# Optimization experiments

Hardware: AMD Instinct MI355X
Metric: run time of the kernel (lower is better)

## Reference

```python
import jax, jax.numpy as jnp
import numpy as np

N0, N1, N2 = 100000, 25000, 6250
F = 128
OUT = 5


def _mean_agg(feat_src, src, dst, n_dst):
    # DGL copy_u + mean: segment mean over destination nodes (0 for isolated dst)
    s = jax.ops.segment_sum(feat_src[src], dst, num_segments=n_dst)
    cnt = jax.ops.segment_sum(jnp.ones_like(dst, dtype=feat_src.dtype), dst, num_segments=n_dst)
    return s / jnp.maximum(cnt, 1.0)[:, None]


def _graph_conv(feat, src, dst, W, b, n):
    # DGL GraphConv, norm='both': D_src^-1/2 gather-sum D_dst^-1/2, then linear
    dt = feat.dtype
    out_deg = jax.ops.segment_sum(jnp.ones_like(src, dtype=dt), src, num_segments=n)
    in_deg = jax.ops.segment_sum(jnp.ones_like(dst, dtype=dt), dst, num_segments=n)
    ns = jnp.where(out_deg > 0, out_deg ** -0.5, 0.0)
    nd = jnp.where(in_deg > 0, in_deg ** -0.5, 0.0)
    agg = jax.ops.segment_sum((feat * ns[:, None])[src], dst, num_segments=n)
    return (agg * nd[:, None]) @ W + b


def setup_inputs() -> dict:
    key = jax.random.key(0)
    keys = jax.random.split(key, 64)
    _c = iter(range(64))
    def nrm(shape, s=0.05):
        return jax.random.normal(keys[next(_c)], shape, dtype=jnp.float32) * s
    def ri(n, hi):
        return jax.random.randint(keys[next(_c)], (n,), 0, hi)
    inp = {
        'X': nrm((N0, 32), 1.0),
        'g0_src': ri(1600000, N0), 'g0_dst': ri(1600000, N0),
        'g1_src': ri(400000, N1), 'g1_dst': ri(400000, N1),
        'g2_src': ri(100000, N2), 'g2_dst': ri(100000, N2),
        'inc0_src': ri(100000, N0), 'inc0_dst': ri(100000, N1),
        'inc1_src': ri(25000, N1), 'inc1_dst': ri(25000, N2),
        'dec0_src': ri(100000, N2), 'dec0_dst': ri(100000, N1),
        'dec1_src': ri(400000, N1), 'dec1_dst': ri(400000, N0),
        'W_emb': nrm((32, F)), 'b_emb': jnp.zeros((F,), jnp.float32),
        'W_gcn0': nrm((F, F)), 'b_gcn0': jnp.zeros((F,), jnp.float32),
        'W_gcn1': nrm((F, F)), 'b_gcn1': jnp.zeros((F,), jnp.float32),
        'W_gcn2': nrm((F, F)), 'b_gcn2': jnp.zeros((F,), jnp.float32),
        'W_enc0': nrm((F, F)), 'b_enc0': jnp.zeros((F,), jnp.float32),
        'W_enc1': nrm((F, F)), 'b_enc1': jnp.zeros((F,), jnp.float32),
        'W_dec0': nrm((F, F)), 'b_dec0': jnp.zeros((F,), jnp.float32),
        'W_dec1': nrm((F, F)), 'b_dec1': jnp.zeros((F,), jnp.float32),
        'W_head0': nrm((2 * F, OUT)), 'b_head0': jnp.zeros((OUT,), jnp.float32),
        'W_head1': nrm((2 * F, OUT)), 'b_head1': jnp.zeros((OUT,), jnp.float32),
        'W_head2': nrm((2 * F, OUT)), 'b_head2': jnp.zeros((OUT,), jnp.float32),
    }
    return inp


def reference(X, g0_src, g0_dst, g1_src, g1_dst, g2_src, g2_dst,
              inc0_src, inc0_dst, inc1_src, inc1_dst,
              dec0_src, dec0_dst, dec1_src, dec1_dst,
              W_emb, b_emb, W_gcn0, b_gcn0, W_gcn1, b_gcn1, W_gcn2, b_gcn2,
              W_enc0, b_enc0, W_enc1, b_enc1, W_dec0, b_dec0, W_dec1, b_dec1,
              W_head0, b_head0, W_head1, b_head1, W_head2, b_head2):
    # embedding at finest scale
    h0 = X @ W_emb + b_emb                                   # [N0, F]
    # encode + pool fine -> coarse (copy_u/mean)
    h1 = _mean_agg(h0 @ W_enc0 + b_enc0, inc0_src, inc0_dst, N1)   # [N1, F]
    h2 = _mean_agg(h1 @ W_enc1 + b_enc1, inc1_src, inc1_dst, N2)   # [N2, F]
    # intra-scale GraphConv
    g0 = _graph_conv(h0, g0_src, g0_dst, W_gcn0, b_gcn0, N0)
    g1 = _graph_conv(h1, g1_src, g1_dst, W_gcn1, b_gcn1, N1)
    g2 = _graph_conv(h2, g2_src, g2_dst, W_gcn2, b_gcn2, N2)
    # decode coarse -> fine
    d2 = g2
    d1 = _mean_agg(d2 @ W_dec0 + b_dec0, dec0_src, dec0_dst, N1)   # [N1, F]
    d0 = _mean_agg(d1 @ W_dec1 + b_dec1, dec1_src, dec1_dst, N0)   # [N0, F]
    # per-scale heads with softmax
    o0 = jax.nn.softmax(jnp.concatenate([g0, d0], -1) @ W_head0 + b_head0, axis=-1)
    o1 = jax.nn.softmax(jnp.concatenate([g1, d1], -1) @ W_head1 + b_head1, axis=-1)
    o2 = jax.nn.softmax(jnp.concatenate([g2, d2], -1) @ W_head2 + b_head2, axis=-1)
    return jnp.concatenate([o0, o1, o2], axis=0)             # [N0+N1+N2, OUT]
```

## Files before the change

### kernel.cpp

```cpp
#include <hip/hip_runtime.h>

#define F 128
static const int N0 = 100000, N1 = 25000, N2 = 6250;

typedef unsigned short u16;
typedef unsigned int   u32;
typedef __attribute__((ext_vector_type(8))) short bf16x8;
typedef __attribute__((ext_vector_type(4))) float f32x4;

__device__ __forceinline__ float bf2f(u16 u) {
    union { u32 i; float f; } v; v.i = ((u32)u) << 16; return v.f;
}
__device__ __forceinline__ u16 f2bf(float f) {
    u32 u = __float_as_uint(f);
    u += 0x7fff + ((u >> 16) & 1);
    return (u16)(u >> 16);
}

struct Seg7 {
    const int* src[7];
    const int* dst[7];
    int end[7];
    int cbase[7];
    int obase[7];
};

#define EPT 4
#define CEPT 8
#define SM32  (64*(32+8)*2 + 128*(32+8)*2 + 128*4)
#define SM128 (64*(128+8)*2 + 128*(128+8)*2 + 128*4)


template <int K, bool AF32, bool MASK>
__device__ __forceinline__ void dev_mm(char* smem, const void* __restrict__ Ap,
                                       const float* __restrict__ W,
                                       const float* __restrict__ bias,
                                       u16* __restrict__ out,
                                       const int* __restrict__ rowptr,
                                       int M, int blk) {
    const int AST = K + 8;
    const int WST = K + 8;
    u16* Al = (u16*)smem;
    u16* Wt = (u16*)(smem + 64 * AST * 2);
    float* bl = (float*)(smem + 64 * AST * 2 + 128 * WST * 2);
    int tid = threadIdx.x;
    int m0 = blk * 64;

    for (int i = tid; i < K * 128; i += 256) {
        int k = i >> 7, n = i & 127;
        Wt[n * WST + k] = f2bf(W[i]);
    }
    for (int i = tid; i < 64 * K; i += 256) {
        int r = i / K, c = i % K;
        int gr = m0 + r;
        u16 v = 0;
        if (gr < M) {
            if (AF32) v = f2bf(((const float*)Ap)[(size_t)gr * K + c]);
            else      v = ((const u16*)Ap)[(size_t)gr * K + c];
        }
        Al[r * AST + c] = v;
    }
    if (tid < 128) bl[tid] = bias[tid];
    __syncthreads();

    int w = tid >> 6;
    int lane = tid & 63;
    int m16 = lane & 15;
    int quad = lane >> 4;

    f32x4 acc[8];
#pragma unroll
    for (int t = 0; t < 8; t++)
#pragma unroll
        for (int r = 0; r < 4; r++) acc[t][r] = 0.f;

    for (int k0 = 0; k0 < K; k0 += 32) {
        bf16x8 af = *(const bf16x8*)&Al[(w * 16 + m16) * AST + k0 + quad * 8];
#pragma unroll
        for (int t = 0; t < 8; t++) {
            bf16x8 bf = *(const bf16x8*)&Wt[(t * 16 + m16) * WST + k0 + quad * 8];
            acc[t] = __builtin_amdgcn_mfma_f32_16x16x32_bf16(af, bf, acc[t], 0, 0, 0);
        }
    }

#pragma unroll
    for (int t = 0; t < 8; t++) {
#pragma unroll
        for (int r = 0; r < 4; r++) {
            int gr = m0 + w * 16 + quad * 4 + r;
            if (gr >= M) continue;
            int gc = t * 16 + m16;
            bool zrow = false;
            if (MASK) zrow = (rowptr[gr + 1] == rowptr[gr]);
            float v = acc[t][r] + bl[gc];
            out[(size_t)gr * F + gc] = zrow ? (u16)0 : f2bf(v);
        }
    }
}

template <int MODE>
__device__ __forceinline__ void dev_gather(const u16* __restrict__ feat,
                                           const int* __restrict__ rowptr,
                                           const int* __restrict__ col,
                                           const int* __restrict__ od,
                                           u16* __restrict__ out, int M, int blk) {
    int wv = (blk * 256 + (int)threadIdx.x) >> 6;
    if (wv >= M) return;
    int lane = threadIdx.x & 63;
    int fo = lane << 1;
    int beg = rowptr[wv], end = rowptr[wv + 1];
    float a0 = 0.f, a1 = 0.f;
    int j = beg;
    for (; j + 8 <= end; j += 8) {
        int cc[8];
#pragma unroll
        for (int t = 0; t < 8; t++) cc[t] = col[j + t];
        float ss[8];
#pragma unroll
        for (int t = 0; t < 8; t++) {
            if (MODE == 1) { int o = od[cc[t]]; ss[t] = o > 0 ? rsqrtf((float)o) : 0.f; }
            else ss[t] = 1.f;
        }
        ushort2 uu[8];
#pragma unroll
        for (int t = 0; t < 8; t++) uu[t] = *(const ushort2*)&feat[(size_t)cc[t] * F + fo];
#pragma unroll
        for (int t = 0; t < 8; t++) { a0 += bf2f(uu[t].x) * ss[t]; a1 += bf2f(uu[t].y) * ss[t]; }
    }
    for (; j < end; j++) {
        int c = col[j];
        float s = 1.f;
        if (MODE == 1) { int o = od[c]; s = o > 0 ? rsqrtf((float)o) : 0.f; }
        ushort2 u = *(const ushort2*)&feat[(size_t)c * F + fo];
        a0 += bf2f(u.x) * s; a1 += bf2f(u.y) * s;
    }
    int deg = end - beg;
    float fs = (MODE == 0) ? (deg > 0 ? 1.f / (float)deg : 0.f)
                           : (deg > 0 ? rsqrtf((float)deg) : 0.f);
    ushort2 o; o.x = f2bf(a0 * fs); o.y = f2bf(a1 * fs);
    *(ushort2*)&out[(size_t)wv * F + fo] = o;
}

template <bool GD>
__device__ __forceinline__ void dev_head(char* smem, const u16* __restrict__ g,
                                         const u16* __restrict__ d,
                                         const int* __restrict__ rowptr,
                                         const int* __restrict__ col,
                                         const float* __restrict__ Wh,
                                         const float* __restrict__ bh,
                                         float* __restrict__ out, int M, int blk) {
    float* Wl = (float*)smem;
    float* bl = (float*)(smem + 1280 * 4);
    int tid = threadIdx.x;
    for (int i = tid; i < 1280; i += 256) Wl[i] = Wh[i];
    if (tid < 5) bl[tid] = bh[tid];
    __syncthreads();

    int lane = tid & 63;
    int wv = tid >> 6;
    int r0 = blk * 32 + wv * 8;
    int k0 = lane << 1;
    for (int i = 0; i < 8; i++) {
        int row = r0 + i;
        if (row < M) {
            float d0v, d1v;
            if (GD) {
                int beg = rowptr[row], end = rowptr[row + 1];
                d0v = 0.f; d1v = 0.f;
                int j = beg;
                for (; j + 4 <= end; j += 4) {
                    int c0 = col[j], c1 = col[j + 1], c2 = col[j + 2], c3 = col[j + 3];
                    ushort2 u0 = *(const ushort2*)&d[(size_t)c0 * F + k0];
                    ushort2 u1 = *(const ushort2*)&d[(size_t)c1 * F + k0];
                    ushort2 u2 = *(const ushort2*)&d[(size_t)c2 * F + k0];
                    ushort2 u3 = *(const ushort2*)&d[(size_t)c3 * F + k0];
                    d0v += bf2f(u0.x) + bf2f(u1.x) + bf2f(u2.x) + bf2f(u3.x);
                    d1v += bf2f(u0.y) + bf2f(u1.y) + bf2f(u2.y) + bf2f(u3.y);
                }
                for (; j < end; j++) {
                    int c = col[j];
                    ushort2 u = *(const ushort2*)&d[(size_t)c * F + k0];
                    d0v += bf2f(u.x); d1v += bf2f(u.y);
                }
                int deg = end - beg;
                float fs = deg > 0 ? 1.f / (float)deg : 0.f;
                d0v *= fs; d1v *= fs;
            } else {
                ushort2 du = *(const ushort2*)&d[(size_t)row * F + k0];
                d0v = bf2f(du.x); d1v = bf2f(du.y);
            }
            ushort2 gu = *(const ushort2*)&g[(size_t)row * F + k0];
            float g0v = bf2f(gu.x), g1v = bf2f(gu.y);
            float p[5];
#pragma unroll
            for (int o = 0; o < 5; o++) {
                p[o] = g0v * Wl[k0 * 5 + o] + g1v * Wl[(k0 + 1) * 5 + o] +
                       d0v * Wl[(k0 + 128) * 5 + o] + d1v * Wl[(k0 + 129) * 5 + o];
            }
#pragma unroll
            for (int o = 0; o < 5; o++) {
                float v = p[o];
                v += __shfl_xor(v, 32, 64);
                v += __shfl_xor(v, 16, 64);
                v += __shfl_xor(v, 8, 64);
                v += __shfl_xor(v, 4, 64);
                v += __shfl_xor(v, 2, 64);
                v += __shfl_xor(v, 1, 64);
                p[o] = v + bl[o];
            }
            if (lane == 0) {
                float m = p[0];
#pragma unroll
                for (int o = 1; o < 5; o++) m = fmaxf(m, p[o]);
                float e[5], s = 0.f;
#pragma unroll
                for (int o = 0; o < 5; o++) { e[o] = expf(p[o] - m); s += e[o]; }
                float inv = 1.f / s;
#pragma unroll
                for (int o = 0; o < 5; o++) out[(size_t)row * 5 + o] = e[o] * inv;
            }
        }
    }
}


__global__ __launch_bounds__(256) void k_count_emb(Seg7 S, int* __restrict__ cnt,
                                                   u16* __restrict__ occ, int ETOT,
                                                   const float* __restrict__ X,
                                                   const float* __restrict__ Wemb,
                                                   const float* __restrict__ bemb,
                                                   u16* __restrict__ h0, int nbMM) {
    __shared__ char smem[SM32];
    if ((int)blockIdx.x < nbMM) {
        dev_mm<32, true, false>(smem, X, Wemb, bemb, h0, nullptr, N0, blockIdx.x);
        return;
    }
    int base = ((int)blockIdx.x - nbMM) * (256 * CEPT) + threadIdx.x;
    int ee[CEPT], grow[CEPT];
#pragma unroll
    for (int t = 0; t < CEPT; t++) {
        int e = base + t * 256;
        ee[t] = e;
        grow[t] = -1;
        if (e < ETOT) {
            int s = 0;
            while (e >= S.end[s]) s++;
            int le = e - ((s == 0) ? 0 : S.end[s - 1]);
            grow[t] = S.cbase[s] + S.dst[s][le];
        }
    }
    u32 r[CEPT];
#pragma unroll
    for (int t = 0; t < CEPT; t++)
        if (grow[t] >= 0) r[t] = atomicAdd((u32*)&cnt[grow[t]], 1u);
#pragma unroll
    for (int t = 0; t < CEPT; t++)
        if (grow[t] >= 0) occ[ee[t]] = (u16)r[t];
}

__global__ __launch_bounds__(256) void k_fill_od(Seg7 S,
                                                 const int* __restrict__ rowptr,
                                                 const u16* __restrict__ occ,
                                                 int* __restrict__ col,
                                                 int* __restrict__ od, int ETOT,
                                                 float invRow, float invOd) {
    int win = blockIdx.x & 7;
    int base = ((int)blockIdx.x >> 3) * (256 * EPT) + threadIdx.x;
#pragma unroll
    for (int t = 0; t < EPT; t++) {
        int e = base + t * 256;
        if (e >= ETOT) break;
        int s = 0;
        while (e >= S.end[s]) s++;
        int le = e - ((s == 0) ? 0 : S.end[s - 1]);
        int grow = S.cbase[s] + S.dst[s][le];
        int w1 = (int)((float)grow * invRow); w1 = w1 > 7 ? 7 : w1;
        int sv = -1;
        if (w1 == win || S.obase[s] >= 0) sv = S.src[s][le];
        if (w1 == win) col[rowptr[grow] + (int)occ[e]] = sv;
        if (S.obase[s] >= 0) {
            int gs = S.obase[s] + sv;
            int w2 = (int)((float)gs * invOd); w2 = w2 > 7 ? 7 : w2;
            if (w2 == win) atomicAdd(&od[gs], 1);
        }
    }
}

#define SCHUNK 4096
__global__ __launch_bounds__(1024) void k_scan1(const int* __restrict__ cnt,
                                                int* __restrict__ partial, int n) {
    __shared__ int red[1024];
    int tid = threadIdx.x;
    int base = blockIdx.x * SCHUNK + tid * 4;
    int s = 0;
#pragma unroll
    for (int j = 0; j < 4; j++) { int i = base + j; if (i < n) s += cnt[i]; }
    red[tid] = s;
    __syncthreads();
    for (int d = 512; d > 0; d >>= 1) {
        if (tid < d) red[tid] += red[tid + d];
        __syncthreads();
    }
    if (tid == 0) partial[blockIdx.x] = red[0];
}

__global__ __launch_bounds__(128) void k_scan2(int* __restrict__ partial, int G) {
    __shared__ int sh[128];
    int tid = threadIdx.x;
    sh[tid] = (tid < G) ? partial[tid] : 0;
    __syncthreads();
    for (int d = 1; d < 128; d <<= 1) {
        int t = (tid >= d) ? sh[tid - d] : 0;
        __syncthreads();
        sh[tid] += t;
        __syncthreads();
    }
    if (tid < G) partial[tid] = (tid > 0) ? sh[tid - 1] : 0;
    if (tid == 127) partial[G] = sh[127];
}

__global__ __launch_bounds__(1024) void k_scan3(const int* __restrict__ cnt,
                                                const int* __restrict__ partial,
                                                int* __restrict__ rowptr,
                                                int n, int G) {
    __shared__ int red[1024];
    int tid = threadIdx.x;
    int base = blockIdx.x * SCHUNK + tid * 4;
    int v0 = 0, v1 = 0, v2 = 0, v3 = 0;
    if (base + 0 < n) v0 = cnt[base + 0];
    if (base + 1 < n) v1 = cnt[base + 1];
    if (base + 2 < n) v2 = cnt[base + 2];
    if (base + 3 < n) v3 = cnt[base + 3];
    red[tid] = v0 + v1 + v2 + v3;
    __syncthreads();
    for (int d = 1; d < 1024; d <<= 1) {
        int t = (tid >= d) ? red[tid - d] : 0;
        __syncthreads();
        red[tid] += t;
        __syncthreads();
    }
    int off = partial[blockIdx.x] + ((tid > 0) ? red[tid - 1] : 0);
    if (base + 0 < n) { rowptr[base + 0] = off; off += v0; }
    if (base + 1 < n) { rowptr[base + 1] = off; off += v1; }
    if (base + 2 < n) { rowptr[base + 2] = off; off += v2; }
    if (base + 3 < n) { rowptr[base + 3] = off; off += v3; }
    if (blockIdx.x == 0 && tid == 0) rowptr[n] = partial[G];
}

template <int MODE>
__global__ __launch_bounds__(256) void k_gather(const u16* __restrict__ feat,
                                                const int* __restrict__ rowptr,
                                                const int* __restrict__ col,
                                                const int* __restrict__ od,
                                                u16* __restrict__ out, int M) {
    dev_gather<MODE>(feat, rowptr, col, od, out, M, blockIdx.x);
}

template <int K, bool AF32, bool MASK>
__global__ __launch_bounds__(256) void k_mm(const void* __restrict__ Ap,
                                            const float* __restrict__ W,
                                            const float* __restrict__ bias,
                                            u16* __restrict__ out,
                                            const int* __restrict__ rowptr,
                                            int M) {
    __shared__ char smem[K == 32 ? SM32 : SM128];
    dev_mm<K, AF32, MASK>(smem, Ap, W, bias, out, rowptr, M, blockIdx.x);
}

template <int MA, int MB>
__global__ __launch_bounds__(256) void k_gather2(
    const u16* fA, const int* rpA, const int* oA, u16* outA, int MAr, int nbA,
    const u16* fB, const int* rpB, const int* oB, u16* outB, int MBr,
    const int* __restrict__ col) {
    if ((int)blockIdx.x < nbA) dev_gather<MA>(fA, rpA, col, oA, outA, MAr, blockIdx.x);
    else                       dev_gather<MB>(fB, rpB, col, oB, outB, MBr, blockIdx.x - nbA);
}

__global__ __launch_bounds__(256) void k_mm2(
    const u16* A1, const float* W1, const float* b1, u16* o1, const int* rp1, int M1, int nb1,
    const u16* A2, const float* W2, const float* b2, u16* o2, int M2) {
    __shared__ char smem[SM128];
    if ((int)blockIdx.x < nb1) dev_mm<128, false, true >(smem, A1, W1, b1, o1, rp1, M1, blockIdx.x);
    else                       dev_mm<128, false, false>(smem, A2, W2, b2, o2, nullptr, M2, blockIdx.x - nb1);
}

__global__ __launch_bounds__(256) void k_head3(
    const u16* Ga, const u16* dFeat, const int* rpD1, const int* colp,
    const float* Wa, const float* Ba, int nb0,
    const u16* Gb, const u16* Db, const float* Wb, const float* Bb, int nb1,
    const u16* Gc, const float* Wc, const float* Bc,
    float* __restrict__ out) {
    __shared__ char smem[1280 * 4 + 32];
    int b = blockIdx.x;
    if (b < nb0)            dev_head<true >(smem, Ga, dFeat, rpD1, colp, Wa, Ba, out, N0, b);
    else if (b < nb0 + nb1) dev_head<false>(smem, Gb, Db, nullptr, nullptr, Wb, Bb, out + (size_t)N0 * 5, N1, b - nb0);
    else                    dev_head<false>(smem, Gc, Gc, nullptr, nullptr, Wc, Bc, out + (size_t)(N0 + N1) * 5, N2, b - nb0 - nb1);
}

extern "C" void kernel_launch(void* const* d_in, const int* in_sizes, int n_in,
                              void* d_out, int out_size, void* d_ws, size_t ws_size,
                              hipStream_t stream) {
    const float* X = (const float*)d_in[0];
    const int *g0s = (const int*)d_in[1], *g0d = (const int*)d_in[2];
    const int *g1s = (const int*)d_in[3], *g1d = (const int*)d_in[4];
    const int *g2s = (const int*)d_in[5], *g2d = (const int*)d_in[6];
    const int *i0s = (const int*)d_in[7], *i0d = (const int*)d_in[8];
    const int *i1s = (const int*)d_in[9], *i1d = (const int*)d_in[10];
    const int *dc0s = (const int*)d_in[11], *dc0d = (const int*)d_in[12];
    const int *dc1s = (const int*)d_in[13], *dc1d = (const int*)d_in[14];
    const float *Wemb = (const float*)d_in[15], *bemb = (const float*)d_in[16];
    const float *Wg0 = (const float*)d_in[17], *bg0 = (const float*)d_in[18];
    const float *Wg1 = (const float*)d_in[19], *bg1 = (const float*)d_in[20];
    const float *Wg2 = (const float*)d_in[21], *bg2 = (const float*)d_in[22];
    const float *We0 = (const float*)d_in[23], *be0 = (const float*)d_in[24];
    const float *We1 = (const float*)d_in[25], *be1 = (const float*)d_in[26];
    const float *Wd0 = (const float*)d_in[27], *bd0 = (const float*)d_in[28];
    const float *Wd1 = (const float*)d_in[29], *bd1 = (const float*)d_in[30];
    const float *Wh0 = (const float*)d_in[31], *bh0 = (const float*)d_in[32];
    const float *Wh1 = (const float*)d_in[33], *bh1 = (const float*)d_in[34];
    const float *Wh2 = (const float*)d_in[35], *bh2 = (const float*)d_in[36];
    const int Eg0 = in_sizes[1], Eg1 = in_sizes[3], Eg2 = in_sizes[5];
    const int Ei0 = in_sizes[7], Ei1 = in_sizes[9];
    const int Ed0 = in_sizes[11], Ed1 = in_sizes[13];
    (void)n_in; (void)out_size; (void)ws_size;

    const int B_I0 = 0;
    const int B_I1 = B_I0 + N1;
    const int B_G2 = B_I1 + N2;
    const int B_D0 = B_G2 + N2;
    const int B_G1 = B_D0 + N1;
    const int B_G0 = B_G1 + N1;
    const int B_D1 = B_G0 + N0;
    const int NROWS = B_D1 + N0;
    const int ETOT  = Eg0 + Eg1 + Eg2 + Ei0 + Ei1 + Ed0 + Ed1;
    const int OB_G0 = 0, OB_G1 = N0, OB_G2 = N0 + N1;
    const int NOD = N0 + N1 + N2;
    const int G = (NROWS + SCHUNK - 1) / SCHUNK;
    const int rowsPerWin = (NROWS + 7) / 8;
    const int odPerWin   = (NOD + 7) / 8;
    const float invRow = 1.0f / (float)rowsPerWin;
    const float invOd  = 1.0f / (float)odPerWin;
    const int NCH = (ETOT + 256 * EPT - 1) / (256 * EPT);

    char* wsb = (char*)d_ws;
    size_t off = 0;
    auto alloc = [&](size_t bytes) -> char* {
        char* p = wsb + off;
        off = (off + bytes + 255) & ~(size_t)255;
        return p;
    };
    u16* h0  = (u16*)alloc((size_t)N0 * F * 2);
    u16* h1  = (u16*)alloc((size_t)N1 * F * 2);
    u16* h2  = (u16*)alloc((size_t)N2 * F * 2);
    u16* G0  = (u16*)alloc((size_t)N0 * F * 2);
    u16* G1  = (u16*)alloc((size_t)N1 * F * 2);
    u16* G2  = (u16*)alloc((size_t)N2 * F * 2);
    u16* D1  = (u16*)alloc((size_t)N1 * F * 2);
    u16* agg = (u16*)alloc((size_t)N0 * F * 2);
    u16* bN1 = (u16*)alloc((size_t)N1 * F * 2);
    u16* bN2 = (u16*)alloc((size_t)N2 * F * 2);
    u16* pA  = D1;
    int* cnt    = (int*)alloc((size_t)NROWS * 4);
    int* od     = (int*)alloc((size_t)NOD * 4);
    int* rowptr = (int*)alloc((size_t)(NROWS + 1) * 4);
    u16* occ    = (u16*)alloc((size_t)ETOT * 2);
    int* col    = (int*)alloc((size_t)ETOT * 4);
    int* part   = (int*)alloc((size_t)(G + 1) * 4);
    float* out = (float*)d_out;

    Seg7 S;
    S.src[0] = i0s;  S.dst[0] = i0d;  S.cbase[0] = B_I0; S.obase[0] = -1;
    S.src[1] = i1s;  S.dst[1] = i1d;  S.cbase[1] = B_I1; S.obase[1] = -1;
    S.src[2] = g2s;  S.dst[2] = g2d;  S.cbase[2] = B_G2; S.obase[2] = OB_G2;
    S.src[3] = dc0s; S.dst[3] = dc0d; S.cbase[3] = B_D0; S.obase[3] = -1;
    S.src[4] = g1s;  S.dst[4] = g1d;  S.cbase[4] = B_G1; S.obase[4] = OB_G1;
    S.src[5] = g0s;  S.dst[5] = g0d;  S.cbase[5] = B_G0; S.obase[5] = OB_G0;
    S.src[6] = dc1s; S.dst[6] = dc1d; S.cbase[6] = B_D1; S.obase[6] = -1;
    {
        int Es[7] = {Ei0, Ei1, Eg2, Ed0, Eg1, Eg0, Ed1};
        int acc = 0;
        for (int i = 0; i < 7; i++) { acc += Es[i]; S.end[i] = acc; }
    }

    const int nbEmb   = (N0 + 63) / 64;
    const int nbCount = (ETOT + 256 * CEPT - 1) / (256 * CEPT);
    const int nbFill  = NCH * 8;

    hipMemsetAsync(cnt, 0, (size_t)((char*)od - (char*)cnt) + (size_t)NOD * 4, stream);
    k_count_emb<<<nbEmb + nbCount, 256, 0, stream>>>(S, cnt, occ, ETOT, X, Wemb, bemb, h0, nbEmb);
    k_scan1<<<G, 1024, 0, stream>>>(cnt, part, NROWS);
    k_scan2<<<1, 128, 0, stream>>>(part, G);
    k_scan3<<<G, 1024, 0, stream>>>(cnt, part, rowptr, NROWS, G);
    k_fill_od<<<nbFill, 256, 0, stream>>>(S, rowptr, occ, col, od, ETOT, invRow, invOd);

    {
        int nbA = (N1 + 3) / 4, nbB = (N0 + 3) / 4;
        k_gather2<0, 1><<<nbA + nbB, 256, 0, stream>>>(
            h0, rowptr + B_I0, nullptr, pA, N1, nbA,
            h0, rowptr + B_G0, od + OB_G0, agg, N0, col);
    }
    {
        int nb1 = (N1 + 63) / 64;
        int nb2 = (N0 + 63) / 64;
        k_mm2<<<nb1 + nb2, 256, 0, stream>>>(pA, We0, be0, h1, rowptr + B_I0, N1, nb1,
                                             agg, Wg0, bg0, G0, N0);
    }
    {
        int nbA = (N2 + 3) / 4, nbB = (N1 + 3) / 4;
        k_gather2<0, 1><<<nbA + nbB, 256, 0, stream>>>(
            h1, rowptr + B_I1, nullptr, bN2, N2, nbA,
            h1, rowptr + B_G1, od + OB_G1, bN1, N1, col);
    }
    {
        int nb1 = (N2 + 63) / 64;
        int nb2 = (N1 + 63) / 64;
        k_mm2<<<nb1 + nb2, 256, 0, stream>>>(bN2, We1, be1, h2, rowptr + B_I1, N2, nb1,
                                             bN1, Wg1, bg1, G1, N1);
    }
    k_gather<1><<<(N2 + 3) / 4, 256, 0, stream>>>(h2, rowptr + B_G2, col, od + OB_G2, bN2, N2);
    k_mm<128, false, false><<<(N2 + 63) / 64, 256, 0, stream>>>(bN2, Wg2, bg2, G2, nullptr, N2);
    k_mm<128, false, false><<<(N2 + 63) / 64, 256, 0, stream>>>(G2, Wd0, bd0, bN2, nullptr, N2);
    k_gather<0><<<(N1 + 3) / 4, 256, 0, stream>>>(bN2, rowptr + B_D0, col, nullptr, D1, N1);
    k_mm<128, false, false><<<(N1 + 63) / 64, 256, 0, stream>>>(D1, Wd1, bd1, bN1, nullptr, N1);
    {
        int nb0 = (N0 + 31) / 32, nb1 = (N1 + 31) / 32, nb2 = (N2 + 31) / 32;
        k_head3<<<nb0 + nb1 + nb2, 256, 0, stream>>>(G0, bN1, rowptr + B_D1, col, Wh0, bh0, nb0,
                                                     G1, D1, Wh1, bh1, nb1,
                                                     G2, Wh2, bh2, out);
    }
}
```

Measured before the change: 745.8 us.

## Fuse sparse gather aggregation into the following MFMA matmul kernels

Replaces the separate gather kernels and matmul kernels with one kernel that gathers 64 aggregated rows per block straight into shared memory, then runs the bf16 MFMA matmul on them. This drops the intermediate global round trip for the aggregated features and removes four kernel launches. In exchange, each block now gathers 64 rows with only four waves, which lowers latency-hiding parallelism for the irregular gather. The per-block weight conversion also now sits on the same critical path as the gather.

```diff
diff --git a/kernel.cpp b/kernel.cpp
--- a/kernel.cpp
+++ b/kernel.cpp
@@ -98,47 +98,108 @@
     }
 }
 
-template <int MODE>
-__device__ __forceinline__ void dev_gather(const u16* __restrict__ feat,
-                                           const int* __restrict__ rowptr,
-                                           const int* __restrict__ col,
-                                           const int* __restrict__ od,
-                                           u16* __restrict__ out, int M, int blk) {
-    int wv = (blk * 256 + (int)threadIdx.x) >> 6;
-    if (wv >= M) return;
-    int lane = threadIdx.x & 63;
+template <int MODE, bool MASK, bool WRITEA>
+__device__ __forceinline__ void dev_mmg(char* smem,
+                                        const u16* __restrict__ feat,
+                                        const int* __restrict__ rowptr,
+                                        const int* __restrict__ col,
+                                        const int* __restrict__ od,
+                                        u16* __restrict__ Aout,
+                                        const float* __restrict__ W,
+                                        const float* __restrict__ bias,
+                                        u16* __restrict__ out, int M, int blk) {
+    const int K = F;
+    const int AST = K + 8;
+    const int WST = K + 8;
+    u16* Al = (u16*)smem;
+    u16* Wt = (u16*)(smem + 64 * AST * 2);
+    float* bl = (float*)(smem + 64 * AST * 2 + 128 * WST * 2);
+    int tid = threadIdx.x;
+    int m0 = blk * 64;
+
+    for (int i = tid; i < K * 128; i += 256) {
+        int k = i >> 7, n = i & 127;
+        Wt[n * WST + k] = f2bf(W[i]);
+    }
+    if (tid < 128) bl[tid] = bias[tid];
+
+    int wv = tid >> 6;
+    int lane = tid & 63;
     int fo = lane << 1;
-    int beg = rowptr[wv], end = rowptr[wv + 1];
-    float a0 = 0.f, a1 = 0.f;
-    int j = beg;
-    for (; j + 8 <= end; j += 8) {
-        int cc[8];
-#pragma unroll
-        for (int t = 0; t < 8; t++) cc[t] = col[j + t];
-        float ss[8];
+    for (int r = wv; r < 64; r += 4) {
+        int row = m0 + r;
+        u16 x0 = 0, x1 = 0;
+        if (row < M) {
+            int beg = rowptr[row], end = rowptr[row + 1];
+            float a0 = 0.f, a1 = 0.f;
+            int j = beg;
+            for (; j + 8 <= end; j += 8) {
+                int cc[8];
+#pragma unroll
+                for (int t = 0; t < 8; t++) cc[t] = col[j + t];
+                float ss[8];
+#pragma unroll
+                for (int t = 0; t < 8; t++) {
+                    if (MODE == 1) { int o = od[cc[t]]; ss[t] = o > 0 ? rsqrtf((float)o) : 0.f; }
+                    else ss[t] = 1.f;
+                }
+                ushort2 uu[8];
+#pragma unroll
+                for (int t = 0; t < 8; t++) uu[t] = *(const ushort2*)&feat[(size_t)cc[t] * F + fo];
+#pragma unroll
+                for (int t = 0; t < 8; t++) { a0 += bf2f(uu[t].x) * ss[t]; a1 += bf2f(uu[t].y) * ss[t]; }
+            }
+            for (; j < end; j++) {
+                int c = col[j];
+                float s = 1.f;
+                if (MODE == 1) { int o = od[c]; s = o > 0 ? rsqrtf((float)o) : 0.f; }
+                ushort2 u = *(const ushort2*)&feat[(size_t)c * F + fo];
+                a0 += bf2f(u.x) * s; a1 += bf2f(u.y) * s;
+            }
+            int deg = end - beg;
+            float fs = (MODE == 0) ? (deg > 0 ? 1.f / (float)deg : 0.f)
+                                   : (deg > 0 ? rsqrtf((float)deg) : 0.f);
+            x0 = f2bf(a0 * fs); x1 = f2bf(a1 * fs);
+        }
+        Al[r * AST + fo] = x0;
+        Al[r * AST + fo + 1] = x1;
+        if (WRITEA && row < M) {
+            ushort2 o; o.x = x0; o.y = x1;
+            *(ushort2*)&Aout[(size_t)row * F + fo] = o;
+        }
+    }
+    __syncthreads();
+
+    int m16 = lane & 15;
+    int quad = lane >> 4;
+    f32x4 acc[8];
+#pragma unroll
+    for (int t = 0; t < 8; t++)
+#pragma unroll
+        for (int r = 0; r < 4; r++) acc[t][r] = 0.f;
+
+    for (int k0 = 0; k0 < K; k0 += 32) {
+        bf16x8 af = *(const bf16x8*)&Al[(wv * 16 + m16) * AST + k0 + quad * 8];
 #pragma unroll
         for (int t = 0; t < 8; t++) {
-            if (MODE == 1) { int o = od[cc[t]]; ss[t] = o > 0 ? rsqrtf((float)o) : 0.f; }
-            else ss[t] = 1.f;
-        }
-        ushort2 uu[8];
-#pragma unroll
-        for (int t = 0; t < 8; t++) uu[t] = *(const ushort2*)&feat[(size_t)cc[t] * F + fo];
-#pragma unroll
-        for (int t = 0; t < 8; t++) { a0 += bf2f(uu[t].x) * ss[t]; a1 += bf2f(uu[t].y) * ss[t]; }
-    }
-    for (; j < end; j++) {
-        int c = col[j];
-        float s = 1.f;
-        if (MODE == 1) { int o = od[c]; s = o > 0 ? rsqrtf((float)o) : 0.f; }
-        ushort2 u = *(const ushort2*)&feat[(size_t)c * F + fo];
-        a0 += bf2f(u.x) * s; a1 += bf2f(u.y) * s;
-    }
-    int deg = end - beg;
-    float fs = (MODE == 0) ? (deg > 0 ? 1.f / (float)deg : 0.f)
-                           : (deg > 0 ? rsqrtf((float)deg) : 0.f);
-    ushort2 o; o.x = f2bf(a0 * fs); o.y = f2bf(a1 * fs);
-    *(ushort2*)&out[(size_t)wv * F + fo] = o;
+            bf16x8 bf = *(const bf16x8*)&Wt[(t * 16 + m16) * WST + k0 + quad * 8];
+            acc[t] = __builtin_amdgcn_mfma_f32_16x16x32_bf16(af, bf, acc[t], 0, 0, 0);
+        }
+    }
+
+#pragma unroll
+    for (int t = 0; t < 8; t++) {
+#pragma unroll
+        for (int r = 0; r < 4; r++) {
+            int gr = m0 + wv * 16 + quad * 4 + r;
+            if (gr >= M) continue;
+            int gc = t * 16 + m16;
+            bool zrow = false;
+            if (MASK) zrow = (rowptr[gr + 1] == rowptr[gr]);
+            float v = acc[t][r] + bl[gc];
+            out[(size_t)gr * F + gc] = zrow ? (u16)0 : f2bf(v);
+        }
+    }
 }
 
 template <bool GD>
@@ -347,15 +408,6 @@
     if (blockIdx.x == 0 && tid == 0) rowptr[n] = partial[G];
 }
 
-template <int MODE>
-__global__ __launch_bounds__(256) void k_gather(const u16* __restrict__ feat,
-                                                const int* __restrict__ rowptr,
-                                                const int* __restrict__ col,
-                                                const int* __restrict__ od,
-                                                u16* __restrict__ out, int M) {
-    dev_gather<MODE>(feat, rowptr, col, od, out, M, blockIdx.x);
-}
-
 template <int K, bool AF32, bool MASK>
 __global__ __launch_bounds__(256) void k_mm(const void* __restrict__ Ap,
                                             const float* __restrict__ W,
@@ -367,21 +419,28 @@
     dev_mm<K, AF32, MASK>(smem, Ap, W, bias, out, rowptr, M, blockIdx.x);
 }
 
-template <int MA, int MB>
-__global__ __launch_bounds__(256) void k_gather2(
-    const u16* fA, const int* rpA, const int* oA, u16* outA, int MAr, int nbA,
-    const u16* fB, const int* rpB, const int* oB, u16* outB, int MBr,
+template <int MODE, bool MASK, bool WRITEA>
+__global__ __launch_bounds__(256) void k_mmg(const u16* __restrict__ feat,
+                                             const int* __restrict__ rowptr,
+                                             const int* __restrict__ col,
+                                             const int* __restrict__ od,
+                                             u16* __restrict__ Aout,
+                                             const float* __restrict__ W,
+                                             const float* __restrict__ bias,
+                                             u16* __restrict__ out, int M) {
+    __shared__ char smem[SM128];
+    dev_mmg<MODE, MASK, WRITEA>(smem, feat, rowptr, col, od, Aout, W, bias, out, M, blockIdx.x);
+}
+
+__global__ __launch_bounds__(256) void k_mmg2(
+    const u16* f1, const int* rp1, const float* W1, const float* b1, u16* o1, int M1, int nb1,
+    const u16* f2, const int* rp2, const int* od2, const float* W2, const float* b2, u16* o2, int M2,
     const int* __restrict__ col) {
-    if ((int)blockIdx.x < nbA) dev_gather<MA>(fA, rpA, col, oA, outA, MAr, blockIdx.x);
-    else                       dev_gather<MB>(fB, rpB, col, oB, outB, MBr, blockIdx.x - nbA);
-}
-
-__global__ __launch_bounds__(256) void k_mm2(
-    const u16* A1, const float* W1, const float* b1, u16* o1, const int* rp1, int M1, int nb1,
-    const u16* A2, const float* W2, const float* b2, u16* o2, int M2) {
     __shared__ char smem[SM128];
-    if ((int)blockIdx.x < nb1) dev_mm<128, false, true >(smem, A1, W1, b1, o1, rp1, M1, blockIdx.x);
-    else                       dev_mm<128, false, false>(smem, A2, W2, b2, o2, nullptr, M2, blockIdx.x - nb1);
+    if ((int)blockIdx.x < nb1)
+        dev_mmg<0, true, false>(smem, f1, rp1, col, nullptr, nullptr, W1, b1, o1, M1, blockIdx.x);
+    else
+        dev_mmg<1, false, false>(smem, f2, rp2, col, od2, nullptr, W2, b2, o2, M2, blockIdx.x - nb1);
 }
 
 __global__ __launch_bounds__(256) void k_head3(
@@ -456,10 +515,8 @@
     u16* G1  = (u16*)alloc((size_t)N1 * F * 2);
     u16* G2  = (u16*)alloc((size_t)N2 * F * 2);
     u16* D1  = (u16*)alloc((size_t)N1 * F * 2);
-    u16* agg = (u16*)alloc((size_t)N0 * F * 2);
     u16* bN1 = (u16*)alloc((size_t)N1 * F * 2);
     u16* bN2 = (u16*)alloc((size_t)N2 * F * 2);
-    u16* pA  = D1;
     int* cnt    = (int*)alloc((size_t)NROWS * 4);
     int* od     = (int*)alloc((size_t)NOD * 4);
     int* rowptr = (int*)alloc((size_t)(NROWS + 1) * 4);
@@ -494,34 +551,20 @@
     k_fill_od<<<nbFill, 256, 0, stream>>>(S, rowptr, occ, col, od, ETOT, invRow, invOd);
 
     {
-        int nbA = (N1 + 3) / 4, nbB = (N0 + 3) / 4;
-        k_gather2<0, 1><<<nbA + nbB, 256, 0, stream>>>(
-            h0, rowptr + B_I0, nullptr, pA, N1, nbA,
-            h0, rowptr + B_G0, od + OB_G0, agg, N0, col);
+        int nb1 = (N1 + 63) / 64, nb2 = (N0 + 63) / 64;
+        k_mmg2<<<nb1 + nb2, 256, 0, stream>>>(h0, rowptr + B_I0, We0, be0, h1, N1, nb1,
+                                              h0, rowptr + B_G0, od + OB_G0, Wg0, bg0, G0, N0, col);
     }
     {
-        int nb1 = (N1 + 63) / 64;
-        int nb2 = (N0 + 63) / 64;
-        k_mm2<<<nb1 + nb2, 256, 0, stream>>>(pA, We0, be0, h1, rowptr + B_I0, N1, nb1,
-                                             agg, Wg0, bg0, G0, N0);
-    }
-    {
-        int nbA = (N2 + 3) / 4, nbB = (N1 + 3) / 4;
-        k_gather2<0, 1><<<nbA + nbB, 256, 0, stream>>>(
-            h1, rowptr + B_I1, nullptr, bN2, N2, nbA,
-            h1, rowptr + B_G1, od + OB_G1, bN1, N1, col);
-    }
-    {
-        int nb1 = (N2 + 63) / 64;
-        int nb2 = (N1 + 63) / 64;
-        k_mm2<<<nb1 + nb2, 256, 0, stream>>>(bN2, We1, be1, h2, rowptr + B_I1, N2, nb1,
-                                             bN1, Wg1, bg1, G1, N1);
-    }
-    k_gather<1><<<(N2 + 3) / 4, 256, 0, stream>>>(h2, rowptr + B_G2, col, od + OB_G2, bN2, N2);
-    k_mm<128, false, false><<<(N2 + 63) / 64, 256, 0, stream>>>(bN2, Wg2, bg2, G2, nullptr, N2);
+        int nb1 = (N2 + 63) / 64, nb2 = (N1 + 63) / 64;
+        k_mmg2<<<nb1 + nb2, 256, 0, stream>>>(h1, rowptr + B_I1, We1, be1, h2, N2, nb1,
+                                              h1, rowptr + B_G1, od + OB_G1, Wg1, bg1, G1, N1, col);
+    }
+    k_mmg<1, false, false><<<(N2 + 63) / 64, 256, 0, stream>>>(
+        h2, rowptr + B_G2, col, od + OB_G2, nullptr, Wg2, bg2, G2, N2);
     k_mm<128, false, false><<<(N2 + 63) / 64, 256, 0, stream>>>(G2, Wd0, bd0, bN2, nullptr, N2);
-    k_gather<0><<<(N1 + 3) / 4, 256, 0, stream>>>(bN2, rowptr + B_D0, col, nullptr, D1, N1);
-    k_mm<128, false, false><<<(N1 + 63) / 64, 256, 0, stream>>>(D1, Wd1, bd1, bN1, nullptr, N1);
+    k_mmg<0, false, true><<<(N1 + 63) / 64, 256, 0, stream>>>(
+        bN2, rowptr + B_D0, col, nullptr, D1, Wd1, bd1, bN1, N1);
     {
         int nb0 = (N0 + 31) / 32, nb1 = (N1 + 31) / 32, nb2 = (N2 + 31) / 32;
         k_head3<<<nb0 + nb1 + nb2, 256, 0, stream>>>(G0, bN1, rowptr + B_D1, col, Wh0, bh0, nb0,
```

Result: slower. 846.0 us (+13.4%).
